# Performance work log

Hardware: AMD Instinct MI355X
Metric: run time of the kernel (lower is better)

Reference implementation:

```python
import jax, jax.numpy as jnp
import numpy as np

# token_type_vocab constants (closed over; original passes a dict)
WORD_TOKEN, SMILES_TOKEN, VALUE_TOKEN, CLS_TOKEN, SEP_TOKEN, MASK_TOKEN = 0, 1, 2, 3, 4, 5
FP_DIM, HID, COL_VOCAB, MAX_POS, TT_VOCAB = 768, 768, 1000, 512, 8
B, S = 64, 512


def setup_inputs() -> dict:
    key = jax.random.key(0)
    ks = jax.random.split(key, 16)
    scale = 0.02
    return {
        "batch_size": B,
        "max_batch_seq_len": S,
        "SMILES_fps": jax.random.normal(ks[0], (B, S, FP_DIM), jnp.float32),
        "word_tokens_ref": jax.random.randint(ks[1], (B, S), 0, COL_VOCAB),
        "values_ref": jax.random.normal(ks[2], (B, S), jnp.float32),
        "token_type_ids": jax.random.randint(ks[3], (B, S), 0, 6),
        "position_ids": jax.random.randint(ks[4], (B, S), 0, MAX_POS),
        "fc1_w": jax.random.normal(ks[5], (FP_DIM, 4 * FP_DIM), jnp.float32) * scale,
        "fc1_b": jnp.zeros((4 * FP_DIM,), jnp.float32),
        "fc2_w": jax.random.normal(ks[6], (4 * FP_DIM, HID), jnp.float32) * scale,
        "fc2_b": jnp.zeros((HID,), jnp.float32),
        "prop_emb": jax.random.normal(ks[7], (COL_VOCAB, HID), jnp.float32) * scale,
        "val_w": jax.random.normal(ks[8], (HID,), jnp.float32) * scale,  # Linear(1, HID) weight
        "val_b": jnp.zeros((HID,), jnp.float32),
        "pos_emb": jax.random.normal(ks[9], (MAX_POS, HID), jnp.float32) * scale,
        "type_emb": jax.random.normal(ks[10], (TT_VOCAB, HID), jnp.float32) * scale,
        "ln_g": jnp.ones((HID,), jnp.float32),
        "ln_b": jnp.zeros((HID,), jnp.float32),
    }


def reference(batch_size, max_batch_seq_len, SMILES_fps, word_tokens_ref, values_ref,
              token_type_ids, position_ids, fc1_w, fc1_b, fc2_w, fc2_b, prop_emb,
              val_w, val_b, pos_emb, type_emb, ln_g, ln_b):
    word_mask = token_type_ids == WORD_TOKEN
    smiles_mask = token_type_ids == SMILES_TOKEN
    value_mask = token_type_ids == VALUE_TOKEN
    # Faithful to source: '&' of mutually exclusive equalities -> always False
    special_mask = (token_type_ids == CLS_TOKEN) & (token_type_ids == SEP_TOKEN) & (token_type_ids == MASK_TOKEN)

    # branch embeddings computed densely, selected per token (masks are disjoint)
    word_e = prop_emb[word_tokens_ref]                                   # [B,S,H]
    smiles_e = jax.nn.relu(jnp.einsum('bsf,fd->bsd', SMILES_fps, fc1_w) + fc1_b)
    smiles_e = jnp.einsum('bsf,fd->bsd', smiles_e, fc2_w) + fc2_b        # [B,S,H]
    value_e = values_ref[..., None] * val_w + val_b                      # [B,S,H]
    special_e = type_emb[token_type_ids]                                 # [B,S,H]

    input_embeddings = jnp.zeros_like(word_e)
    input_embeddings = jnp.where(word_mask[..., None], word_e, input_embeddings)
    input_embeddings = jnp.where(smiles_mask[..., None], smiles_e, input_embeddings)
    input_embeddings = jnp.where(value_mask[..., None], value_e, input_embeddings)
    input_embeddings = jnp.where(special_mask[..., None], special_e, input_embeddings)

    emb = input_embeddings + pos_emb[position_ids] + type_emb[token_type_ids]
    mu = jnp.mean(emb, axis=-1, keepdims=True)
    var = jnp.mean(jnp.square(emb - mu), axis=-1, keepdims=True)
    emb = (emb - mu) * jax.lax.rsqrt(var + 1e-12) * ln_g + ln_b
    return emb  # dropout_rate=0 (eval): identity
```

## Files before the change

kernel.cpp:

```cpp
#include <hip/hip_runtime.h>
#include <hip/hip_bf16.h>
#include <stdint.h>


typedef __bf16 bf16x8 __attribute__((ext_vector_type(8)));
typedef float f32x4 __attribute__((ext_vector_type(4)));

__device__ __forceinline__ unsigned short f2bf(float f) {
  union { float f; unsigned int u; } c; c.f = f;
  unsigned int u = c.u;
  return (unsigned short)((u + 0x7FFFu + ((u >> 16) & 1u)) >> 16);
}
__device__ __forceinline__ float bf2f(unsigned short b) {
  union { unsigned int u; float f; } c; c.u = ((unsigned int)b) << 16;
  return c.f;
}

__global__ __launch_bounds__(256) void k_prep(
    const float* __restrict__ fc1_w, const float* __restrict__ fc2_w,
    unsigned short* __restrict__ w1t, unsigned short* __restrict__ w2t,
    int* __restrict__ counter) {
  if (blockIdx.x == 0 && threadIdx.x == 0) *counter = 0;
  __shared__ float tile[32][33];
  int b = blockIdx.x;
  const float* src;
  unsigned short* dst;
  int R, C, bx, by;
  if (b < 2304) {
    src = fc1_w; dst = w1t; R = 768; C = 3072;
    bx = (b % 96) * 32; by = (b / 96) * 32;
  } else {
    b -= 2304;
    src = fc2_w; dst = w2t; R = 3072; C = 768;
    bx = (b % 24) * 32; by = (b / 24) * 32;
  }
  int tx = threadIdx.x & 31;
  int ty = threadIdx.x >> 5;
#pragma unroll
  for (int i = 0; i < 4; i++) {
    int r = by + ty + i * 8;
    tile[ty + i * 8][tx] = src[(size_t)r * C + bx + tx];
  }
  __syncthreads();
#pragma unroll
  for (int i = 0; i < 4; i++) {
    int c = bx + ty + i * 8;
    dst[(size_t)c * R + by + tx] = f2bf(tile[tx][ty + i * 8]);
  }
}

__global__ void k_compact(const int* __restrict__ tt, int* __restrict__ counter,
                          int* __restrict__ idx, int* __restrict__ slot, int BS) {
  int t = blockIdx.x * 256 + threadIdx.x;
  if (t >= BS) return;
  if (tt[t] == 1) {
    int s = atomicAdd(counter, 1);
    idx[s] = t;
    slot[t] = s;
  }
}

__global__ __launch_bounds__(256) void k_gather(
    const float* __restrict__ fps, const int* __restrict__ idx,
    const int* __restrict__ counter, unsigned short* __restrict__ A1, int cap) {
  int wave = threadIdx.x >> 6, lane = threadIdx.x & 63;
  int s = blockIdx.x * 4 + wave;
  int n = *counter;
  int n_pad = (n + 127) & ~127;
  if (n_pad > cap) n_pad = cap;
  if (s >= n_pad) return;
  ushort4* dst = (ushort4*)(A1 + (size_t)s * 768);
  if (s < n) {
    const float4* srcr = (const float4*)(fps + (size_t)idx[s] * 768);
#pragma unroll
    for (int i = 0; i < 3; i++) {
      float4 v = srcr[lane + (i << 6)];
      ushort4 o;
      o.x = f2bf(v.x); o.y = f2bf(v.y); o.z = f2bf(v.z); o.w = f2bf(v.w);
      dst[lane + (i << 6)] = o;
    }
  } else {
    ushort4 z = {0, 0, 0, 0};
#pragma unroll
    for (int i = 0; i < 3; i++) dst[lane + (i << 6)] = z;
  }
}

template <int MODE, int NB, int KS, int AST, int BST>
__global__ __launch_bounds__(256) void k_gemm(
    const unsigned short* __restrict__ A,
    const unsigned short* __restrict__ BT,
    const float* __restrict__ bias,
    unsigned short* __restrict__ C,
    const int* __restrict__ counter, int N, int cap) {
  int n = *counter;
  int n_pad = (n + 127) & ~127;
  if (n_pad > cap) n_pad = cap;
  const int mb = n_pad >> 7;

  constexpr int NCOL = NB * KS;
  constexpr int C_CH = (KS == 4) ? 4 : 2;
  constexpr int A_CH = 8 / C_CH;
  constexpr int CLEN = NCOL / C_CH;

  const int bid = blockIdx.x;
  const int xcd = bid & 7;
  const int j = bid >> 3;
  const int mc = xcd / C_CH, cc = xcd % C_CH;
  const int q = mb / A_CH, r = mb % A_CH;
  const int mlen = q + (mc < r ? 1 : 0);
  const int mbase = mc * q + (mc < r ? mc : r);
  if (j >= mlen * CLEN) return;
  const int m_blk = mbase + j / CLEN;
  const int c_blk = cc * CLEN + j % CLEN;
  const int ks = c_blk / NB;
  const int nb = c_blk % NB;
  const int m0 = m_blk * 128, n0 = nb * 128;
  const int k0g = ks * 768;

  __shared__ __attribute__((aligned(128))) char smem[65536];
  auto lds = (__attribute__((address_space(3))) char*)smem;

  const int t = threadIdx.x;
  const int wave = t >> 6;
  const int lane = t & 63;
  const int wm = (wave >> 1) * 64;
  const int wn = (wave & 1) * 64;

  f32x4 acc[4][4] = {};

  auto stage = [&](int kk0, int bufbase) {
#pragma unroll
    for (int i = 0; i < 4; i++) {
      int c = i * 256 + t;
      int rr = c >> 3;
      int k8 = (c & 7) ^ (rr & 7);
      const unsigned short* ga = A + (size_t)(m0 + rr) * AST + kk0 + k8 * 8;
      __builtin_amdgcn_global_load_lds(
          (const __attribute__((address_space(1))) void*)ga,
          (__attribute__((address_space(3))) void*)(lds + bufbase + i * 4096 + wave * 1024),
          16, 0, 0);
    }
#pragma unroll
    for (int i = 0; i < 4; i++) {
      int c = i * 256 + t;
      int rr = c >> 3;
      int k8 = (c & 7) ^ (rr & 7);
      const unsigned short* gb = BT + (size_t)(n0 + rr) * BST + kk0 + k8 * 8;
      __builtin_amdgcn_global_load_lds(
          (const __attribute__((address_space(1))) void*)gb,
          (__attribute__((address_space(3))) void*)(lds + bufbase + 16384 + i * 4096 + wave * 1024),
          16, 0, 0);
    }
  };

  stage(k0g, 0);
  __syncthreads();
  int cur = 0;

  for (int it = 0; it < 12; ++it) {
    if (it + 1 < 12) stage(k0g + (it + 1) * 64, (cur ^ 1) * 32768);
    const int bufbase = cur * 32768;
#pragma unroll
    for (int kk = 0; kk < 2; kk++) {
      bf16x8 af[4], bfr[4];
      int kbyte = (kk * 32 + ((lane >> 4) * 8)) * 2;
#pragma unroll
      for (int mi = 0; mi < 4; mi++) {
        int rr = wm + mi * 16 + (lane & 15);
        af[mi] = *(const bf16x8*)(smem + bufbase + rr * 128 + (kbyte ^ ((rr & 7) << 4)));
      }
#pragma unroll
      for (int ni = 0; ni < 4; ni++) {
        int rr = wn + ni * 16 + (lane & 15);
        bfr[ni] = *(const bf16x8*)(smem + bufbase + 16384 + rr * 128 + (kbyte ^ ((rr & 7) << 4)));
      }
#pragma unroll
      for (int mi = 0; mi < 4; mi++)
#pragma unroll
        for (int ni = 0; ni < 4; ni++)
          acc[mi][ni] = __builtin_amdgcn_mfma_f32_16x16x32_bf16(
              af[mi], bfr[ni], acc[mi][ni], 0, 0, 0);
    }
    __syncthreads();
    cur ^= 1;
  }

#pragma unroll
  for (int ni = 0; ni < 4; ni++) {
    int col = n0 + wn + ni * 16 + (lane & 15);
    float bv = (MODE == 1) ? bias[col] : 0.f;
#pragma unroll
    for (int mi = 0; mi < 4; mi++) {
#pragma unroll
      for (int j2 = 0; j2 < 4; j2++) {
        int row = m0 + wm + mi * 16 + ((lane >> 4) * 4) + j2;
        float v = acc[mi][ni][j2] + bv;
        if constexpr (MODE == 1) {
          v = v > 0.f ? v : 0.f;
          C[(size_t)row * N + col] = f2bf(v);
        } else {
          C[((size_t)ks * cap + row) * N + col] = f2bf(v);
        }
      }
    }
  }
}

template <int KS>
__global__ __launch_bounds__(256) void k_assemble(
    const unsigned short* __restrict__ sout, const float* __restrict__ fc2b,
    const int* __restrict__ slot,
    const int* __restrict__ ttid, const int* __restrict__ word,
    const float* __restrict__ values, const int* __restrict__ posid,
    const float* __restrict__ prop, const float* __restrict__ valw,
    const float* __restrict__ valb, const float* __restrict__ pose,
    const float* __restrict__ tye, const float* __restrict__ lng,
    const float* __restrict__ lnb, float* __restrict__ out, int BS, int cap) {
  int wave = threadIdx.x >> 6, lane = threadIdx.x & 63;
  int t = blockIdx.x * 4 + wave;
  if (t >= BS) return;
  int tt = ttid[t];

  float v[12];
  if (tt == 1) {
    int sl = slot[t];
    const ushort4* pr[KS];
#pragma unroll
    for (int p = 0; p < KS; p++)
      pr[p] = (const ushort4*)(sout + ((size_t)p * cap + sl) * 768);
    const float4* b4 = (const float4*)fc2b;
#pragma unroll
    for (int i = 0; i < 3; i++) {
      float4 b = b4[lane + (i << 6)];
      float a0 = b.x, a1 = b.y, a2 = b.z, a3 = b.w;
#pragma unroll
      for (int p = 0; p < KS; p++) {
        ushort4 u = pr[p][lane + (i << 6)];
        a0 += bf2f(u.x); a1 += bf2f(u.y); a2 += bf2f(u.z); a3 += bf2f(u.w);
      }
      v[4 * i] = a0; v[4 * i + 1] = a1; v[4 * i + 2] = a2; v[4 * i + 3] = a3;
    }
  } else if (tt == 0) {
    const float4* row = (const float4*)(prop + (size_t)word[t] * 768);
#pragma unroll
    for (int i = 0; i < 3; i++) {
      float4 x = row[lane + (i << 6)];
      v[4 * i] = x.x; v[4 * i + 1] = x.y; v[4 * i + 2] = x.z; v[4 * i + 3] = x.w;
    }
  } else if (tt == 2) {
    float val = values[t];
#pragma unroll
    for (int i = 0; i < 3; i++) {
      float4 w = ((const float4*)valw)[lane + (i << 6)];
      float4 b = ((const float4*)valb)[lane + (i << 6)];
      v[4 * i] = val * w.x + b.x; v[4 * i + 1] = val * w.y + b.y;
      v[4 * i + 2] = val * w.z + b.z; v[4 * i + 3] = val * w.w + b.w;
    }
  } else {
#pragma unroll
    for (int j = 0; j < 12; j++) v[j] = 0.f;
  }

  const float4* p4 = (const float4*)(pose + (size_t)posid[t] * 768);
  const float4* ty4 = (const float4*)(tye + (size_t)tt * 768);
#pragma unroll
  for (int i = 0; i < 3; i++) {
    float4 p = p4[lane + (i << 6)];
    float4 y = ty4[lane + (i << 6)];
    v[4 * i] += p.x + y.x; v[4 * i + 1] += p.y + y.y;
    v[4 * i + 2] += p.z + y.z; v[4 * i + 3] += p.w + y.w;
  }

  float s = 0.f;
#pragma unroll
  for (int j = 0; j < 12; j++) s += v[j];
#pragma unroll
  for (int o = 32; o >= 1; o >>= 1) s += __shfl_xor(s, o);
  float mu = s * (1.0f / 768.0f);

  float qv = 0.f;
#pragma unroll
  for (int j = 0; j < 12; j++) { float d = v[j] - mu; qv += d * d; }
#pragma unroll
  for (int o = 32; o >= 1; o >>= 1) qv += __shfl_xor(qv, o);
  float rs = 1.0f / sqrtf(qv * (1.0f / 768.0f) + 1e-12f);

  float4* o4 = (float4*)(out + (size_t)t * 768);
#pragma unroll
  for (int i = 0; i < 3; i++) {
    float4 g = ((const float4*)lng)[lane + (i << 6)];
    float4 b = ((const float4*)lnb)[lane + (i << 6)];
    float4 r;
    r.x = (v[4 * i] - mu) * rs * g.x + b.x;
    r.y = (v[4 * i + 1] - mu) * rs * g.y + b.y;
    r.z = (v[4 * i + 2] - mu) * rs * g.z + b.z;
    r.w = (v[4 * i + 3] - mu) * rs * g.w + b.w;
    o4[lane + (i << 6)] = r;
  }
}

extern "C" void kernel_launch(void* const* d_in, const int* in_sizes, int n_in,
                              void* d_out, int out_size, void* d_ws, size_t ws_size,
                              hipStream_t stream) {
  const int BS = in_sizes[3];
  const float* fps    = (const float*)d_in[2];
  const int*   word   = (const int*)d_in[3];
  const float* values = (const float*)d_in[4];
  const int*   tt     = (const int*)d_in[5];
  const int*   pos    = (const int*)d_in[6];
  const float* fc1_w  = (const float*)d_in[7];
  const float* fc1_b  = (const float*)d_in[8];
  const float* fc2_w  = (const float*)d_in[9];
  const float* fc2_b  = (const float*)d_in[10];
  const float* prop   = (const float*)d_in[11];
  const float* valw   = (const float*)d_in[12];
  const float* valb   = (const float*)d_in[13];
  const float* pose   = (const float*)d_in[14];
  const float* tye    = (const float*)d_in[15];
  const float* lng    = (const float*)d_in[16];
  const float* lnb    = (const float*)d_in[17];
  float* out = (float*)d_out;

  char* ws = (char*)d_ws;
  const size_t off_idx  = 256;
  const size_t off_slot = off_idx + (size_t)BS * 4;
  const size_t off_w1t  = off_slot + (size_t)BS * 4;
  const size_t off_w2t  = off_w1t + (size_t)768 * 3072 * 2;
  const size_t off_A1   = off_w2t + (size_t)3072 * 768 * 2;
  const size_t fixed    = off_A1;
  size_t avail = ws_size > fixed ? ws_size - fixed : 0;

  const size_t per_tok4 = 768 * 2 + 3072 * 2 + 4 * 768 * 2;
  const bool splitk = avail >= (size_t)8192 * per_tok4;

  int cap;
  if (splitk) {
    cap = 8192;
  } else {
    const size_t per_tok1 = 768 * 2 + 3072 * 2 + 768 * 2;
    long c = (long)(avail / per_tok1);
    c &= ~511L;
    if (c > BS) c = BS;
    if (c < 512) c = 512;
    cap = (int)c;
  }
  const int MBcap = cap / 128;

  const size_t off_h1   = off_A1 + (size_t)cap * 768 * 2;
  const size_t off_sout = off_h1 + (size_t)cap * 3072 * 2;

  int* counter = (int*)(ws + 0);
  int* idx     = (int*)(ws + off_idx);
  int* slot    = (int*)(ws + off_slot);
  unsigned short* w1t = (unsigned short*)(ws + off_w1t);
  unsigned short* w2t = (unsigned short*)(ws + off_w2t);
  unsigned short* A1  = (unsigned short*)(ws + off_A1);
  unsigned short* h1  = (unsigned short*)(ws + off_h1);
  unsigned short* sout = (unsigned short*)(ws + off_sout);

  k_prep<<<4608, 256, 0, stream>>>(fc1_w, fc2_w, w1t, w2t, counter);
  k_compact<<<(BS + 255) / 256, 256, 0, stream>>>(tt, counter, idx, slot, BS);
  k_gather<<<cap / 4, 256, 0, stream>>>(fps, idx, counter, A1, cap);

  k_gemm<1, 24, 1, 768, 768><<<24 * MBcap, 256, 0, stream>>>(
      A1, w1t, fc1_b, h1, counter, 3072, cap);

  if (splitk) {
    k_gemm<0, 6, 4, 3072, 3072><<<24 * MBcap, 256, 0, stream>>>(
        h1, w2t, nullptr, sout, counter, 768, cap);
    k_assemble<4><<<(BS + 3) / 4, 256, 0, stream>>>(
        sout, fc2_b, slot, tt, word, values, pos, prop, valw, valb, pose, tye,
        lng, lnb, out, BS, cap);
  } else {
    k_gemm<0, 6, 1, 3072, 3072><<<6 * MBcap, 256, 0, stream>>>(
        h1, w2t, nullptr, sout, counter, 768, cap);
    k_assemble<1><<<(BS + 3) / 4, 256, 0, stream>>>(
        sout, fc2_b, slot, tt, word, values, pos, prop, valw, valb, pose, tye,
        lng, lnb, out, BS, cap);
  }
}
```

Before: 124.6 us.

## Fuse SMILES row gather and bf16 conversion into first GEMM; refine pipeline waits

Removes the separate gather kernel and the A1 staging buffer. The first GEMM now loads fp32 fingerprint rows through the compacted index directly into registers, converts them to bf16 and writes them to LDS, while B still streams via global_load_lds. Both GEMMs replace __syncthreads with explicit vmcnt/lgkmcnt waits and raw barriers so the next tile's loads stay in flight during compute. This saves one launch and one write-plus-read of the gathered matrix. In exchange the first GEMM reads fp32 A repeatedly across the column blocks and uses more registers.

Measured after the change: 139.0 us. 1.12x slower.

```diff
diff --git a/kernel.cpp b/kernel.cpp
--- a/kernel.cpp
+++ b/kernel.cpp
@@ -14,6 +14,16 @@
 __device__ __forceinline__ float bf2f(unsigned short b) {
   union { unsigned int u; float f; } c; c.u = ((unsigned int)b) << 16;
   return c.f;
+}
+__device__ __forceinline__ unsigned pk2(float a, float b) {
+  return (unsigned)f2bf(a) | ((unsigned)f2bf(b) << 16);
+}
+__device__ __forceinline__ void barrier_sync() {
+  asm volatile("" ::: "memory");
+  __builtin_amdgcn_sched_barrier(0);
+  __builtin_amdgcn_s_barrier();
+  __builtin_amdgcn_sched_barrier(0);
+  asm volatile("" ::: "memory");
 }
 
 __global__ __launch_bounds__(256) void k_prep(
@@ -60,39 +70,158 @@
   }
 }
 
-__global__ __launch_bounds__(256) void k_gather(
+__global__ __launch_bounds__(256) void k_gemm1(
     const float* __restrict__ fps, const int* __restrict__ idx,
-    const int* __restrict__ counter, unsigned short* __restrict__ A1, int cap) {
-  int wave = threadIdx.x >> 6, lane = threadIdx.x & 63;
-  int s = blockIdx.x * 4 + wave;
+    const unsigned short* __restrict__ BT,
+    const float* __restrict__ bias,
+    unsigned short* __restrict__ C,
+    const int* __restrict__ counter, int cap) {
   int n = *counter;
   int n_pad = (n + 127) & ~127;
   if (n_pad > cap) n_pad = cap;
-  if (s >= n_pad) return;
-  ushort4* dst = (ushort4*)(A1 + (size_t)s * 768);
-  if (s < n) {
-    const float4* srcr = (const float4*)(fps + (size_t)idx[s] * 768);
-#pragma unroll
-    for (int i = 0; i < 3; i++) {
-      float4 v = srcr[lane + (i << 6)];
-      ushort4 o;
-      o.x = f2bf(v.x); o.y = f2bf(v.y); o.z = f2bf(v.z); o.w = f2bf(v.w);
-      dst[lane + (i << 6)] = o;
-    }
-  } else {
-    ushort4 z = {0, 0, 0, 0};
-#pragma unroll
-    for (int i = 0; i < 3; i++) dst[lane + (i << 6)] = z;
-  }
-}
-
-template <int MODE, int NB, int KS, int AST, int BST>
-__global__ __launch_bounds__(256) void k_gemm(
+  const int mb = n_pad >> 7;
+
+  const int bid = blockIdx.x;
+  const int xcd = bid & 7;
+  const int j = bid >> 3;
+  const int mc = xcd >> 1, cc = xcd & 1;
+  const int q = mb >> 2, r = mb & 3;
+  const int mlen = q + (mc < r ? 1 : 0);
+  const int mbase = mc * q + (mc < r ? mc : r);
+  if (j >= mlen * 12) return;
+  const int m_blk = mbase + j / 12;
+  const int nb = cc * 12 + j % 12;
+  const int m0 = m_blk * 128, n0 = nb * 128;
+
+  __shared__ __attribute__((aligned(128))) char smem[65536];
+  auto lds = (__attribute__((address_space(3))) char*)smem;
+  const int t = threadIdx.x;
+  const int wave = t >> 6, lane = t & 63;
+  const int wm = (wave >> 1) * 64, wn = (wave & 1) * 64;
+
+  const float* arow[4];
+  bool avalid[4];
+#pragma unroll
+  for (int i = 0; i < 4; i++) {
+    int c = i * 256 + t;
+    int rr = c >> 3;
+    int koff = ((c & 7) ^ (rr & 7)) << 3;
+    int grow = m0 + rr;
+    avalid[i] = grow < n;
+    arow[i] = fps + (size_t)(avalid[i] ? idx[grow] : 0) * 768 + koff;
+  }
+
+  f32x4 acc[4][4] = {};
+  float4 av[4][2];
+
+  auto loadA = [&](int kt) {
+#pragma unroll
+    for (int i = 0; i < 4; i++) {
+      if (avalid[i]) {
+        const float4* p = (const float4*)(arow[i] + kt * 64);
+        av[i][0] = p[0];
+        av[i][1] = p[1];
+      } else {
+        av[i][0] = make_float4(0.f, 0.f, 0.f, 0.f);
+        av[i][1] = make_float4(0.f, 0.f, 0.f, 0.f);
+      }
+    }
+  };
+  auto stageB = [&](int kt, int bufbase) {
+#pragma unroll
+    for (int i = 0; i < 4; i++) {
+      int c = i * 256 + t;
+      int rr = c >> 3;
+      const unsigned short* gb =
+          BT + (size_t)(n0 + rr) * 768 + kt * 64 + (((c & 7) ^ (rr & 7)) << 3);
+      __builtin_amdgcn_global_load_lds(
+          (const __attribute__((address_space(1))) void*)gb,
+          (__attribute__((address_space(3))) void*)(lds + bufbase + 16384 +
+                                                    i * 4096 + wave * 1024),
+          16, 0, 0);
+    }
+  };
+  auto writeA = [&](int bufbase) {
+#pragma unroll
+    for (int i = 0; i < 4; i++) {
+      int c = i * 256 + t;
+      uint4 w;
+      w.x = pk2(av[i][0].x, av[i][0].y);
+      w.y = pk2(av[i][0].z, av[i][0].w);
+      w.z = pk2(av[i][1].x, av[i][1].y);
+      w.w = pk2(av[i][1].z, av[i][1].w);
+      *(uint4*)(smem + bufbase + c * 16) = w;
+    }
+  };
+  auto compute = [&](int bufbase) {
+#pragma unroll
+    for (int kk = 0; kk < 2; kk++) {
+      bf16x8 af[4], bfr[4];
+      int kbyte = (kk * 32 + ((lane >> 4) * 8)) * 2;
+#pragma unroll
+      for (int mi = 0; mi < 4; mi++) {
+        int rr = wm + mi * 16 + (lane & 15);
+        af[mi] = *(const bf16x8*)(smem + bufbase + rr * 128 + (kbyte ^ ((rr & 7) << 4)));
+      }
+#pragma unroll
+      for (int ni = 0; ni < 4; ni++) {
+        int rr = wn + ni * 16 + (lane & 15);
+        bfr[ni] = *(const bf16x8*)(smem + bufbase + 16384 + rr * 128 + (kbyte ^ ((rr & 7) << 4)));
+      }
+#pragma unroll
+      for (int mi = 0; mi < 4; mi++)
+#pragma unroll
+        for (int ni = 0; ni < 4; ni++)
+          acc[mi][ni] = __builtin_amdgcn_mfma_f32_16x16x32_bf16(
+              af[mi], bfr[ni], acc[mi][ni], 0, 0, 0);
+    }
+  };
+
+  loadA(0);
+  stageB(0, 0);
+  writeA(0);
+  asm volatile("s_waitcnt lgkmcnt(0)" ::: "memory");
+
+  for (int it = 0; it < 12; ++it) {
+    const int cur = it & 1, nxt = cur ^ 1;
+    if (it + 1 < 12) {
+      loadA(it + 1);
+      stageB(it + 1, nxt * 32768);
+      __builtin_amdgcn_sched_barrier(0);
+      asm volatile("s_waitcnt vmcnt(12)" ::: "memory");
+    } else {
+      asm volatile("s_waitcnt vmcnt(0)" ::: "memory");
+    }
+    barrier_sync();
+    compute(cur * 32768);
+    if (it + 1 < 12) writeA(nxt * 32768);
+    asm volatile("s_waitcnt lgkmcnt(0)" ::: "memory");
+    barrier_sync();
+  }
+
+#pragma unroll
+  for (int ni = 0; ni < 4; ni++) {
+    int col = n0 + wn + ni * 16 + (lane & 15);
+    float bv = bias[col];
+#pragma unroll
+    for (int mi = 0; mi < 4; mi++) {
+#pragma unroll
+      for (int j2 = 0; j2 < 4; j2++) {
+        int row = m0 + wm + mi * 16 + ((lane >> 4) * 4) + j2;
+        float v = acc[mi][ni][j2] + bv;
+        v = v > 0.f ? v : 0.f;
+        C[(size_t)row * 3072 + col] = f2bf(v);
+      }
+    }
+  }
+}
+
+template <int NB, int KS>
+__global__ __launch_bounds__(256) void k_gemm2(
     const unsigned short* __restrict__ A,
     const unsigned short* __restrict__ BT,
-    const float* __restrict__ bias,
     unsigned short* __restrict__ C,
-    const int* __restrict__ counter, int N, int cap) {
+    const int* __restrict__ counter, int cap) {
   int n = *counter;
   int n_pad = (n + 127) & ~127;
   if (n_pad > cap) n_pad = cap;
@@ -120,22 +249,19 @@
 
   __shared__ __attribute__((aligned(128))) char smem[65536];
   auto lds = (__attribute__((address_space(3))) char*)smem;
-
   const int t = threadIdx.x;
-  const int wave = t >> 6;
-  const int lane = t & 63;
-  const int wm = (wave >> 1) * 64;
-  const int wn = (wave & 1) * 64;
+  const int wave = t >> 6, lane = t & 63;
+  const int wm = (wave >> 1) * 64, wn = (wave & 1) * 64;
 
   f32x4 acc[4][4] = {};
 
-  auto stage = [&](int kk0, int bufbase) {
+  auto stage = [&](int kt, int bufbase) {
 #pragma unroll
     for (int i = 0; i < 4; i++) {
       int c = i * 256 + t;
       int rr = c >> 3;
-      int k8 = (c & 7) ^ (rr & 7);
-      const unsigned short* ga = A + (size_t)(m0 + rr) * AST + kk0 + k8 * 8;
+      int k8 = ((c & 7) ^ (rr & 7)) << 3;
+      const unsigned short* ga = A + (size_t)(m0 + rr) * 3072 + k0g + kt * 64 + k8;
       __builtin_amdgcn_global_load_lds(
           (const __attribute__((address_space(1))) void*)ga,
           (__attribute__((address_space(3))) void*)(lds + bufbase + i * 4096 + wave * 1024),
@@ -145,8 +271,8 @@
     for (int i = 0; i < 4; i++) {
       int c = i * 256 + t;
       int rr = c >> 3;
-      int k8 = (c & 7) ^ (rr & 7);
-      const unsigned short* gb = BT + (size_t)(n0 + rr) * BST + kk0 + k8 * 8;
+      int k8 = ((c & 7) ^ (rr & 7)) << 3;
+      const unsigned short* gb = BT + (size_t)(n0 + rr) * 3072 + k0g + kt * 64 + k8;
       __builtin_amdgcn_global_load_lds(
           (const __attribute__((address_space(1))) void*)gb,
           (__attribute__((address_space(3))) void*)(lds + bufbase + 16384 + i * 4096 + wave * 1024),
@@ -154,17 +280,22 @@
     }
   };
 
-  stage(k0g, 0);
-  __syncthreads();
-  int cur = 0;
-
+  stage(0, 0);
   for (int it = 0; it < 12; ++it) {
-    if (it + 1 < 12) stage(k0g + (it + 1) * 64, (cur ^ 1) * 32768);
-    const int bufbase = cur * 32768;
+    const int cur = it & 1, nxt = cur ^ 1;
+    if (it + 1 < 12) {
+      stage(it + 1, nxt * 32768);
+      __builtin_amdgcn_sched_barrier(0);
+      asm volatile("s_waitcnt vmcnt(8)" ::: "memory");
+    } else {
+      asm volatile("s_waitcnt vmcnt(0)" ::: "memory");
+    }
+    barrier_sync();
 #pragma unroll
     for (int kk = 0; kk < 2; kk++) {
       bf16x8 af[4], bfr[4];
       int kbyte = (kk * 32 + ((lane >> 4) * 8)) * 2;
+      const int bufbase = cur * 32768;
 #pragma unroll
       for (int mi = 0; mi < 4; mi++) {
         int rr = wm + mi * 16 + (lane & 15);
@@ -182,26 +313,19 @@
           acc[mi][ni] = __builtin_amdgcn_mfma_f32_16x16x32_bf16(
               af[mi], bfr[ni], acc[mi][ni], 0, 0, 0);
     }
-    __syncthreads();
-    cur ^= 1;
+    asm volatile("s_waitcnt lgkmcnt(0)" ::: "memory");
+    barrier_sync();
   }
 
 #pragma unroll
   for (int ni = 0; ni < 4; ni++) {
     int col = n0 + wn + ni * 16 + (lane & 15);
-    float bv = (MODE == 1) ? bias[col] : 0.f;
 #pragma unroll
     for (int mi = 0; mi < 4; mi++) {
 #pragma unroll
       for (int j2 = 0; j2 < 4; j2++) {
         int row = m0 + wm + mi * 16 + ((lane >> 4) * 4) + j2;
-        float v = acc[mi][ni][j2] + bv;
-        if constexpr (MODE == 1) {
-          v = v > 0.f ? v : 0.f;
-          C[(size_t)row * N + col] = f2bf(v);
-        } else {
-          C[((size_t)ks * cap + row) * N + col] = f2bf(v);
-        }
+        C[((size_t)ks * cap + row) * 768 + col] = f2bf(acc[mi][ni][j2]);
       }
     }
   }
@@ -327,18 +451,18 @@
   const size_t off_slot = off_idx + (size_t)BS * 4;
   const size_t off_w1t  = off_slot + (size_t)BS * 4;
   const size_t off_w2t  = off_w1t + (size_t)768 * 3072 * 2;
-  const size_t off_A1   = off_w2t + (size_t)3072 * 768 * 2;
-  const size_t fixed    = off_A1;
+  const size_t off_h1   = off_w2t + (size_t)3072 * 768 * 2;
+  const size_t fixed    = off_h1;
   size_t avail = ws_size > fixed ? ws_size - fixed : 0;
 
-  const size_t per_tok4 = 768 * 2 + 3072 * 2 + 4 * 768 * 2;
+  const size_t per_tok4 = 3072 * 2 + 4 * 768 * 2;
   const bool splitk = avail >= (size_t)8192 * per_tok4;
 
   int cap;
   if (splitk) {
     cap = 8192;
   } else {
-    const size_t per_tok1 = 768 * 2 + 3072 * 2 + 768 * 2;
+    const size_t per_tok1 = 3072 * 2 + 768 * 2;
     long c = (long)(avail / per_tok1);
     c &= ~511L;
     if (c > BS) c = BS;
@@ -347,7 +471,6 @@
   }
   const int MBcap = cap / 128;
 
-  const size_t off_h1   = off_A1 + (size_t)cap * 768 * 2;
   const size_t off_sout = off_h1 + (size_t)cap * 3072 * 2;
 
   int* counter = (int*)(ws + 0);
@@ -355,26 +478,21 @@
   int* slot    = (int*)(ws + off_slot);
   unsigned short* w1t = (unsigned short*)(ws + off_w1t);
   unsigned short* w2t = (unsigned short*)(ws + off_w2t);
-  unsigned short* A1  = (unsigned short*)(ws + off_A1);
   unsigned short* h1  = (unsigned short*)(ws + off_h1);
   unsigned short* sout = (unsigned short*)(ws + off_sout);
 
   k_prep<<<4608, 256, 0, stream>>>(fc1_w, fc2_w, w1t, w2t, counter);
   k_compact<<<(BS + 255) / 256, 256, 0, stream>>>(tt, counter, idx, slot, BS);
-  k_gather<<<cap / 4, 256, 0, stream>>>(fps, idx, counter, A1, cap);
-
-  k_gemm<1, 24, 1, 768, 768><<<24 * MBcap, 256, 0, stream>>>(
-      A1, w1t, fc1_b, h1, counter, 3072, cap);
+
+  k_gemm1<<<24 * MBcap, 256, 0, stream>>>(fps, idx, w1t, fc1_b, h1, counter, cap);
 
   if (splitk) {
-    k_gemm<0, 6, 4, 3072, 3072><<<24 * MBcap, 256, 0, stream>>>(
-        h1, w2t, nullptr, sout, counter, 768, cap);
+    k_gemm2<6, 4><<<24 * MBcap, 256, 0, stream>>>(h1, w2t, sout, counter, cap);
     k_assemble<4><<<(BS + 3) / 4, 256, 0, stream>>>(
         sout, fc2_b, slot, tt, word, values, pos, prop, valw, valb, pose, tye,
         lng, lnb, out, BS, cap);
   } else {
-    k_gemm<0, 6, 1, 3072, 3072><<<6 * MBcap, 256, 0, stream>>>(
-        h1, w2t, nullptr, sout, counter, 768, cap);
+    k_gemm2<6, 1><<<6 * MBcap, 256, 0, stream>>>(h1, w2t, sout, counter, cap);
     k_assemble<1><<<(BS + 3) / 4, 256, 0, stream>>>(
         sout, fc2_b, slot, tt, word, values, pos, prop, valw, valb, pose, tye,
         lng, lnb, out, BS, cap);
```
